# Kernel tuning notes

Hardware: AMD Instinct MI355X
Metric: run time of the kernel (lower is better)

## Reference

```python
import jax, jax.numpy as jnp
import numpy as np

B, N, D, H, DFF, L = 2, 1024, 384, 8, 512, 4
HD = D // H  # 48
RBF_COUNT, RBF_MIN, RBF_MAX = 16, 0.0, 20.0


def layer_norm(x, g, b, eps=1e-5):
    m = jnp.mean(x, axis=-1, keepdims=True)
    v = jnp.var(x, axis=-1, keepdims=True)
    return (x - m) / jnp.sqrt(v + eps) * g + b


def setup_inputs() -> dict:
    key = jax.random.key(0)
    ks = jax.random.split(key, 30)
    rn = lambda k, shape, s=0.02: (jax.random.normal(k, shape, jnp.float32) * s)
    inp = {
        'x_rigid': jax.random.normal(ks[0], (B, N, D), jnp.float32),
        'altered_direction': jax.random.normal(ks[1], (B, N, N, 3), jnp.float32),
        'orientation': jax.random.normal(ks[2], (B, N, N, 3, 3), jnp.float32),
        'distance': jax.random.uniform(ks[3], (B, N, N), jnp.float32) * RBF_MAX,
        'attention_mask': jax.random.randint(ks[4], (B, N, N), 0, 2).astype(jnp.int32),
        'Wq': rn(ks[5], (L, D, D)), 'bq': rn(ks[6], (L, D)),
        'Wk': rn(ks[7], (L, D, D)), 'bk': rn(ks[8], (L, D)),
        'Wv': rn(ks[9], (L, D, D)), 'bv': rn(ks[10], (L, D)),
        'W3': rn(ks[11], (L, D, 3)), 'b3': rn(ks[12], (L, 3)),
        'Wmlp': rn(ks[13], (L, RBF_COUNT), 0.1), 'bmlp': rn(ks[14], (L,), 0.1),
        'Wfc': rn(ks[15], (L, D + 3, D)), 'bfc': rn(ks[16], (L, D)),
        'Wff1': rn(ks[17], (L, D, DFF)), 'bff1': rn(ks[18], (L, DFF)),
        'Wff2': rn(ks[19], (L, DFF, D)), 'bff2': rn(ks[20], (L, D)),
        'ln1_g': jnp.ones((L, D), jnp.float32), 'ln1_b': jnp.zeros((L, D), jnp.float32),
        'ln2_g': jnp.ones((L, D), jnp.float32), 'ln2_b': jnp.zeros((L, D), jnp.float32),
    }
    return inp


def reference(x_rigid, altered_direction, orientation, distance, attention_mask,
              Wq, bq, Wk, bk, Wv, bv, W3, b3, Wmlp, bmlp, Wfc, bfc,
              Wff1, bff1, Wff2, bff2, ln1_g, ln1_b, ln2_g, ln2_b):
    # RBF features of pairwise distance: [B,N,N,16] (shared across layers)
    mu = jnp.linspace(RBF_MIN, RBF_MAX, RBF_COUNT).astype(x_rigid.dtype)
    sigma = (RBF_MAX - RBF_MIN) / RBF_COUNT
    rbf = jnp.exp(-(((distance[..., None] - mu) / sigma) ** 2))
    mask0 = attention_mask == 0  # [B,N,N]
    scale = jnp.sqrt(jnp.asarray(HD, x_rigid.dtype))

    x = x_rigid
    for l in range(L):
        h = layer_norm(x, ln1_g[l], ln1_b[l])
        q = (h @ Wq[l] + bq[l]).reshape(B, N, H, HD).transpose(0, 2, 1, 3)
        k = (h @ Wk[l] + bk[l]).reshape(B, N, H, HD).transpose(0, 2, 1, 3)
        v = (h @ Wv[l] + bv[l]).reshape(B, N, H, HD).transpose(0, 2, 1, 3)
        scores = jnp.einsum('bhqd,bhkd->bhqk', q, k) / scale
        # RBF distance bias via 16->1 linear (head-broadcast, same as repeat+mlp)
        dis = jnp.einsum('bqkr,r->bqk', rbf, Wmlp[l]) + bmlp[l]
        scores = scores + dis[:, None]
        scores = jnp.where(mask0[:, None], jnp.asarray(-1e9, scores.dtype), scores)
        attn = jax.nn.softmax(scores, axis=-1)
        attn_v = jnp.einsum('bhqk,bhkd->bhqd', attn, v)
        attn_v = attn_v.transpose(0, 2, 1, 3).reshape(B, N, D)
        # merged-head softmax drives the geometric frame update
        merged = jax.nn.softmax(jnp.sum(scores, axis=1), axis=-1)  # [B,N,N]
        v3d = h @ W3[l] + b3[l]  # [B,N,3]
        v3d_map = jnp.einsum('bijmn,bjn->bijn', orientation, v3d)  # [B,N,N,3]
        v3d_dir = jnp.cross(altered_direction, v3d_map)  # [B,N,N,3]
        attn_frame = jnp.mean(merged[..., None] * v3d_dir, axis=-2)  # [B,N,3]
        out = jnp.concatenate([attn_v, attn_frame], axis=-1) @ Wfc[l] + bfc[l]
        x = x + out
        h2 = layer_norm(x, ln2_g[l], ln2_b[l])
        x = x + (jax.nn.relu(h2 @ Wff1[l] + bff1[l]) @ Wff2[l] + bff2[l])
    return x
```

## Files before the change

kernel.cpp:

```cpp
#include <hip/hip_runtime.h>
#include <math.h>

constexpr int B_ = 2, N_ = 1024, D_ = 384, H_ = 8, HD_ = 48, DFF2 = 512, L_ = 4;
constexpr int BN_ = B_ * N_;
constexpr size_t NNs = (size_t)N_ * N_;
constexpr size_t BNNc = (size_t)B_ * N_ * N_;
constexpr int JT = 64, NSPLIT = 4;
constexpr int CCLD = 448;
constexpr float RSCALE = 0.14433756729740643f;

typedef short bf16x8 __attribute__((ext_vector_type(8)));
typedef float f32x4 __attribute__((ext_vector_type(4)));

__device__ inline float wsum(float v) {
#pragma unroll
  for (int m = 32; m; m >>= 1) v += __shfl_xor(v, m, 64);
  return v;
}
__device__ inline float b2f(unsigned int s) {
  union { unsigned int u; float f; } v; v.u = s << 16; return v.f;
}
__device__ inline unsigned short f2b(float f) {
  union { float f; unsigned int u; } v; v.f = f;
  unsigned int r = v.u + 0x7fffu + ((v.u >> 16) & 1u);
  return (unsigned short)(r >> 16);
}

__global__ __launch_bounds__(256) void misc_kernel(float* __restrict__ x,
                                                   const float* __restrict__ x_rigid,
                                                   unsigned short* __restrict__ qp,
                                                   unsigned short* __restrict__ kpf,
                                                   const float* __restrict__ bq,
                                                   const float* __restrict__ bk,
                                                   const float* __restrict__ bv,
                                                   float* __restrict__ bqkv) {
  int gid = blockIdx.x * 256 + threadIdx.x;
  if (gid < 786432) { x[gid] = x_rigid[gid]; return; }
  gid -= 786432;
  if (gid < 262144) {
    int r = gid >> 7, rem = gid & 127;
    int h = rem >> 4, c = rem & 15;
    qp[(size_t)r * 512 + h * 64 + 48 + c] = 0;
    return;
  }
  gid -= 262144;
  if (gid < 262144) {
    int fh = gid >> 8, rem = gid & 255;
    kpf[(size_t)fh * 1024 + 768 + rem] = 0;
    return;
  }
  gid -= 262144;
  if (gid < L_ * 1152) {
    int l = gid / 1152, n = gid % 1152;
    bqkv[gid] = (n < 384) ? bq[l * D_ + n] : (n < 768) ? bk[l * D_ + n - 384] : bv[l * D_ + n - 768];
  }
}

__global__ __launch_bounds__(256) void pack_all_kernel(
    const float* __restrict__ Wq, const float* __restrict__ Wk, const float* __restrict__ Wv,
    const float* __restrict__ Wfc, const float* __restrict__ Wff1, const float* __restrict__ Wff2,
    unsigned short* __restrict__ WqkvT, unsigned short* __restrict__ WfcT,
    unsigned short* __restrict__ Wff1T, unsigned short* __restrict__ Wff2T) {
  __shared__ float ts[32][33];
  const int bid = blockIdx.x;
  const int lz = blockIdx.z;
  const int t = threadIdx.x;
  const float* in;
  unsigned short* out;
  size_t istr, ostr;
  int K, Nc, Kpad, n0, k0;
  if (bid < 432) {
    int which = bid / 144, r = bid % 144;
    n0 = (r % 12) * 32; k0 = (r / 12) * 32;
    in = (which == 0) ? Wq : (which == 1) ? Wk : Wv;
    istr = (size_t)D_ * D_;
    out = WqkvT + (size_t)which * 384 * 384;
    ostr = (size_t)1152 * D_;
    K = D_; Nc = D_; Kpad = D_;
  } else if (bid < 600) {
    int r = bid - 432;
    n0 = (r % 12) * 32; k0 = (r / 12) * 32;
    in = Wfc; istr = (size_t)387 * D_;
    out = WfcT; ostr = (size_t)D_ * CCLD;
    K = 387; Nc = D_; Kpad = CCLD;
  } else if (bid < 792) {
    int r = bid - 600;
    n0 = (r % 16) * 32; k0 = (r / 16) * 32;
    in = Wff1; istr = (size_t)D_ * DFF2;
    out = Wff1T; ostr = (size_t)DFF2 * D_;
    K = D_; Nc = DFF2; Kpad = D_;
  } else {
    int r = bid - 792;
    n0 = (r % 12) * 32; k0 = (r / 16 == 0 ? 0 : 0, r / 12) * 32;
    in = Wff2; istr = (size_t)DFF2 * D_;
    out = Wff2T; ostr = (size_t)D_ * DFF2;
    K = DFF2; Nc = D_; Kpad = DFF2;
  }
  const float* inl = in + (size_t)lz * istr;
  unsigned short* outl = out + (size_t)lz * ostr;
#pragma unroll
  for (int u = 0; u < 4; ++u) {
    int i = t + u * 256, kk = i >> 5, nn = i & 31;
    int k = k0 + kk;
    ts[kk][nn] = (k < K) ? inl[(size_t)k * Nc + n0 + nn] : 0.f;
  }
  __syncthreads();
#pragma unroll
  for (int u = 0; u < 4; ++u) {
    int i = t + u * 256, nn = i >> 5, kk = i & 31;
    outl[(size_t)(n0 + nn) * Kpad + k0 + kk] = f2b(ts[kk][nn]);
  }
}

__global__ __launch_bounds__(256) void precomp_kernel(const float* __restrict__ ori,
                                                      const float* __restrict__ ad,
                                                      const float* __restrict__ dist,
                                                      const int* __restrict__ mask,
                                                      const float* __restrict__ Wmlp,
                                                      const float* __restrict__ bmlp,
                                                      uint2* __restrict__ Ga,
                                                      unsigned int* __restrict__ Gz,
                                                      unsigned short* __restrict__ db4) {
  size_t i4 = ((size_t)blockIdx.x * 256 + threadIdx.x) * 4;
  if (i4 >= BNNc) return;
  float ov[36], av[12];
  const float4* op4 = reinterpret_cast<const float4*>(ori + i4 * 9);
#pragma unroll
  for (int u = 0; u < 9; ++u) {
    float4 v = op4[u];
    ov[u * 4 + 0] = v.x; ov[u * 4 + 1] = v.y; ov[u * 4 + 2] = v.z; ov[u * 4 + 3] = v.w;
  }
  const float4* ap4 = reinterpret_cast<const float4*>(ad + i4 * 3);
#pragma unroll
  for (int u = 0; u < 3; ++u) {
    float4 v = ap4[u];
    av[u * 4 + 0] = v.x; av[u * 4 + 1] = v.y; av[u * 4 + 2] = v.z; av[u * 4 + 3] = v.w;
  }
  float4 dv4 = *reinterpret_cast<const float4*>(dist + i4);
  int4 mk4 = *reinterpret_cast<const int4*>(mask + i4);
  float dvs[4] = {dv4.x, dv4.y, dv4.z, dv4.w};
  int mks[4] = {mk4.x, mk4.y, mk4.z, mk4.w};
  uint4 gaout[2];
  unsigned int gzout[4];
#pragma unroll
  for (int e = 0; e < 4; ++e) {
    const float* op = &ov[e * 9];
    const float* ap = &av[e * 3];
    float c0 = op[0] + op[3] + op[6];
    float c1 = op[1] + op[4] + op[7];
    float c2 = op[2] + op[5] + op[8];
    float a0 = ap[0], a1 = ap[1], a2 = ap[2];
    unsigned int w0 = (unsigned int)f2b(a1 * c2) | ((unsigned int)f2b(a2 * c1) << 16);
    unsigned int w1 = (unsigned int)f2b(a2 * c0) | ((unsigned int)f2b(a0 * c2) << 16);
    ((unsigned int*)gaout)[e * 2 + 0] = w0;
    ((unsigned int*)gaout)[e * 2 + 1] = w1;
    gzout[e] = (unsigned int)f2b(a0 * c1) | ((unsigned int)f2b(a1 * c0) << 16);
  }
  *reinterpret_cast<uint4*>(&Ga[i4]) = gaout[0];
  *reinterpret_cast<uint4*>(&Ga[i4 + 2]) = gaout[1];
  *reinterpret_cast<uint4*>(&Gz[i4]) = *reinterpret_cast<uint4*>(gzout);
  float sv[4][4];
#pragma unroll
  for (int e = 0; e < 4; ++e) {
    float rb[16];
#pragma unroll
    for (int r = 0; r < 16; ++r) {
      float tt = (dvs[e] - (float)r * (20.0f / 15.0f)) * 0.8f;
      rb[r] = __expf(-tt * tt);
    }
#pragma unroll
    for (int l2 = 0; l2 < L_; ++l2) {
      float s = bmlp[l2];
#pragma unroll
      for (int r = 0; r < 16; ++r) s += rb[r] * Wmlp[l2 * 16 + r];
      sv[e][l2] = s;
    }
  }
#pragma unroll
  for (int l2 = 0; l2 < L_; ++l2) {
    unsigned int lo = (unsigned int)f2b(mks[0] == 0 ? -1e9f : sv[0][l2]) |
                      ((unsigned int)f2b(mks[1] == 0 ? -1e9f : sv[1][l2]) << 16);
    unsigned int hi = (unsigned int)f2b(mks[2] == 0 ? -1e9f : sv[2][l2]) |
                      ((unsigned int)f2b(mks[3] == 0 ? -1e9f : sv[3][l2]) << 16);
    uint2 w; w.x = lo; w.y = hi;
    *reinterpret_cast<uint2*>(&db4[(size_t)l2 * BNNc + i4]) = w;
  }
}

__global__ __launch_bounds__(256) void geomb_kernel(const float* __restrict__ ori,
                                                    const float* __restrict__ ad,
                                                    uint2* __restrict__ Ga,
                                                    unsigned int* __restrict__ Gz) {
  size_t i = (size_t)blockIdx.x * 256 + threadIdx.x;
  size_t stride = (size_t)gridDim.x * 256;
  for (; i < BNNc; i += stride) {
    const float* op = ori + i * 9;
    const float* ap = ad + i * 3;
    float c0 = op[0] + op[3] + op[6];
    float c1 = op[1] + op[4] + op[7];
    float c2 = op[2] + op[5] + op[8];
    float a0 = ap[0], a1 = ap[1], a2 = ap[2];
    uint2 oa;
    oa.x = (unsigned int)f2b(a1 * c2) | ((unsigned int)f2b(a2 * c1) << 16);
    oa.y = (unsigned int)f2b(a2 * c0) | ((unsigned int)f2b(a0 * c2) << 16);
    Ga[i] = oa;
    Gz[i] = (unsigned int)f2b(a0 * c1) | ((unsigned int)f2b(a1 * c0) << 16);
  }
}
__global__ __launch_bounds__(256) void rbf4_kernel(const float* __restrict__ dist,
                                                   const int* __restrict__ mask,
                                                   const float* __restrict__ Wmlp,
                                                   const float* __restrict__ bmlp,
                                                   unsigned short* __restrict__ db4) {
  size_t i = (size_t)blockIdx.x * 256 + threadIdx.x;
  size_t stride = (size_t)gridDim.x * 256;
  for (; i < BNNc; i += stride) {
    float dv = dist[i];
    bool msk = (mask[i] == 0);
    float rb[16];
#pragma unroll
    for (int r = 0; r < 16; ++r) {
      float tt = (dv - (float)r * (20.0f / 15.0f)) * 0.8f;
      rb[r] = __expf(-tt * tt);
    }
#pragma unroll
    for (int l2 = 0; l2 < L_; ++l2) {
      float sv = bmlp[l2];
#pragma unroll
      for (int r = 0; r < 16; ++r) sv += rb[r] * Wmlp[l2 * 16 + r];
      db4[(size_t)l2 * BNNc + i] = f2b(msk ? -1e9f : sv);
    }
  }
}
__global__ __launch_bounds__(256) void rbf_kernel(const float* __restrict__ dist,
                                                  const int* __restrict__ mask,
                                                  const float* __restrict__ wm,
                                                  const float* __restrict__ bm,
                                                  unsigned short* __restrict__ dbias) {
  size_t i = (size_t)blockIdx.x * 256 + threadIdx.x;
  size_t stride = (size_t)gridDim.x * 256;
  float w[16];
#pragma unroll
  for (int r = 0; r < 16; ++r) w[r] = wm[r];
  float b0 = bm[0];
  for (; i < BNNc; i += stride) {
    float dv = dist[i];
    float sv = b0;
#pragma unroll
    for (int r = 0; r < 16; ++r) {
      float tt = (dv - (float)r * (20.0f / 15.0f)) * 0.8f;
      sv += __expf(-tt * tt) * w[r];
    }
    dbias[i] = f2b((mask[i] == 0) ? -1e9f : sv);
  }
}

template <bool V3D>
__global__ __launch_bounds__(256) void ln_kernel(const float* __restrict__ x,
                                                 const float* __restrict__ g,
                                                 const float* __restrict__ b,
                                                 unsigned short* __restrict__ out,
                                                 const float* __restrict__ W3,
                                                 const float* __restrict__ b3,
                                                 float* __restrict__ v3d) {
  int lane = threadIdx.x & 63, wid = threadIdx.x >> 6;
  int row = blockIdx.x * 4 + wid;
  const float* xp = x + (size_t)row * D_;
  float v[6], s = 0.f, s2 = 0.f;
#pragma unroll
  for (int i = 0; i < 6; ++i) {
    v[i] = xp[lane + i * 64];
    s += v[i]; s2 += v[i] * v[i];
  }
  s = wsum(s); s2 = wsum(s2);
  float mean = s * (1.0f / D_);
  float var = s2 * (1.0f / D_) - mean * mean;
  float rstd = rsqrtf(var + 1e-5f);
  unsigned short* op = out + (size_t)row * D_;
  float a0 = 0.f, a1 = 0.f, a2 = 0.f;
#pragma unroll
  for (int i = 0; i < 6; ++i) {
    int d = lane + i * 64;
    float nv = (v[i] - mean) * rstd * g[d] + b[d];
    op[d] = f2b(nv);
    if (V3D) {
      a0 += nv * W3[d * 3 + 0];
      a1 += nv * W3[d * 3 + 1];
      a2 += nv * W3[d * 3 + 2];
    }
  }
  if (V3D) {
    a0 = wsum(a0); a1 = wsum(a1); a2 = wsum(a2);
    if (lane == 0) {
      v3d[row * 3 + 0] = a0 + b3[0];
      v3d[row * 3 + 1] = a1 + b3[1];
      v3d[row * 3 + 2] = a2 + b3[2];
    }
  }
}

template <int EPI>
__global__ __launch_bounds__(256) void mfma_gemm2(const unsigned short* __restrict__ A, int lda,
                                                  const unsigned short* __restrict__ WT, int ldw,
                                                  const float* __restrict__ bias,
                                                  float* __restrict__ C0, float* __restrict__ C1,
                                                  float* __restrict__ C2, int ldc, int K) {
  __shared__ __align__(16) unsigned short As[2][64 * 72];
  __shared__ __align__(16) unsigned short Bs[2][32 * 72];
  const int t = threadIdx.x;
  const int l = t & 63, w = t >> 6;
  const int lr = l & 15, lk = l >> 4;
  const int n0 = blockIdx.x * 32, m0 = blockIdx.y * 64;
  const int wm = (w & 1) * 32, wn = (w >> 1) * 16;
  const int arow = t >> 3, acol8 = (t & 7) * 8;
  uint4 ra0, ra1, rb;
  const unsigned short* pa0 = A + (size_t)(m0 + arow) * lda + acol8;
  const unsigned short* pa1 = A + (size_t)(m0 + arow + 32) * lda + acol8;
  const unsigned short* pb = WT + (size_t)(n0 + arow) * ldw + acol8;
  ra0 = *reinterpret_cast<const uint4*>(pa0);
  ra1 = *reinterpret_cast<const uint4*>(pa1);
  rb = *reinterpret_cast<const uint4*>(pb);
  f32x4 acc[2] = {};
  int p = 0;
  for (int kt = 0; kt < K; kt += 64) {
    *reinterpret_cast<uint4*>(&As[p][arow * 72 + acol8]) = ra0;
    *reinterpret_cast<uint4*>(&As[p][(arow + 32) * 72 + acol8]) = ra1;
    *reinterpret_cast<uint4*>(&Bs[p][arow * 72 + acol8]) = rb;
    if (kt + 64 < K) {
      ra0 = *reinterpret_cast<const uint4*>(pa0 + kt + 64);
      ra1 = *reinterpret_cast<const uint4*>(pa1 + kt + 64);
      rb = *reinterpret_cast<const uint4*>(pb + kt + 64);
    }
    __syncthreads();
#pragma unroll
    for (int ks = 0; ks < 2; ++ks) {
      bf16x8 av0 = *reinterpret_cast<const bf16x8*>(&As[p][(wm + lr) * 72 + ks * 32 + lk * 8]);
      bf16x8 av1 = *reinterpret_cast<const bf16x8*>(&As[p][(wm + 16 + lr) * 72 + ks * 32 + lk * 8]);
      bf16x8 bv = *reinterpret_cast<const bf16x8*>(&Bs[p][(wn + lr) * 72 + ks * 32 + lk * 8]);
      acc[0] = __builtin_amdgcn_mfma_f32_16x16x32_bf16(av0, bv, acc[0], 0, 0, 0);
      acc[1] = __builtin_amdgcn_mfma_f32_16x16x32_bf16(av1, bv, acc[1], 0, 0, 0);
    }
    p ^= 1;
  }
#pragma unroll
  for (int mi = 0; mi < 2; ++mi)
#pragma unroll
    for (int e = 0; e < 4; ++e) {
      int row = m0 + wm + mi * 16 + lk * 4 + e;
      int col = n0 + wn + lr;
      float v = acc[mi][e] + bias[col];
      if (EPI == 0) {
        if (col < 384) {
          int h = col / 48, hd = col - h * 48;
          ((unsigned short*)C0)[(size_t)row * 512 + h * 64 + hd] = f2b(v * RSCALE);
        } else if (col < 768) {
          int c2 = col - 384;
          int h = c2 / 48, d = c2 - h * 48;
          int b2 = row >> 10, j = row & 1023;
          int jb = j >> 4, jr = j & 15;
          int ks = d >> 5, dd = d & 31;
          size_t fid = (((size_t)(b2 * 64 + jb) * 8 + h) << 1) + ks;
          ((unsigned short*)C1)[fid * 512 + (size_t)(jr + ((dd >> 3) << 4)) * 8 + (d & 7)] = f2b(v);
        } else {
          int d = col - 768;
          int b2 = row >> 10, j = row & 1023;
          int jg = j >> 5, df = d >> 4;
          size_t fid = (size_t)(b2 * 32 + jg) * 24 + df;
          ((unsigned short*)C2)[fid * 512 + (size_t)((d & 15) + (((j & 31) >> 3) << 4)) * 8 + (j & 7)] = f2b(v);
        }
      }
      if (EPI == 1) C0[(size_t)row * ldc + col] += v;
      if (EPI == 2) ((unsigned short*)C0)[(size_t)row * ldc + col] = f2b(fmaxf(v, 0.f));
    }
}

template <bool USEG>
__global__ __launch_bounds__(512, 4) void attn16_kernel(
    const unsigned short* __restrict__ qp, const unsigned short* __restrict__ kpf,
    const unsigned short* __restrict__ vf, const unsigned short* __restrict__ db_l,
    const uint2* __restrict__ Ga, const unsigned int* __restrict__ Gz,
    const float* __restrict__ ad, const float* __restrict__ ori,
    const float* __restrict__ v3d,
    unsigned short* __restrict__ pO, float* __restrict__ pM, float* __restrict__ pL,
    float* __restrict__ pF, float* __restrict__ pMg, float* __restrict__ pLg) {
  __shared__ __align__(16) unsigned short pbuf[8 * 16 * 72];
  __shared__ __align__(16) unsigned short msw[8 * 16 * 68];
  __shared__ __align__(16) float dbs[16 * 68];
  __shared__ float fg_s[16];

  const int t = threadIdx.x;
  const int wv = t >> 6, l = t & 63;
  const int lr = l & 15, lk = l >> 4;
  const int sgrp = blockIdx.y;
  const int i0 = blockIdx.x * 16;
  const int b = i0 >> 10, ib = i0 & 1023;
  const int mr = t >> 5, mc = t & 31;

  const bf16x8 qf0 = *reinterpret_cast<const bf16x8*>(
      qp + (size_t)(i0 + lr) * 512 + wv * 64 + lk * 8);
  const bf16x8 qf1 = *reinterpret_cast<const bf16x8*>(
      qp + (size_t)(i0 + lr) * 512 + wv * 64 + 32 + lk * 8);

  f32x4 Ofr[3] = {};
  float fracc[2][3] = {};
  float m_ph[4], l_ph[4], fhv[4];
#pragma unroll
  for (int e = 0; e < 4; ++e) { m_ph[e] = -INFINITY; l_ph[e] = 0.f; }
  float m_mg = -INFINITY, l_mg = 0.f;

  for (int jt = sgrp * (N_ / NSPLIT); jt < (sgrp + 1) * (N_ / NSPLIT); jt += JT) {
    uint2 ga_r0, ga_r1;
    unsigned int gz_r0, gz_r1;
    float w0p = 0.f, w1p = 0.f, w2p = 0.f;
    if (USEG) {
      const float* vp = v3d + (size_t)((b << 10) + jt + l) * 3;
      w0p = vp[0]; w1p = vp[1]; w2p = vp[2];
      size_t pij0 = ((size_t)b * N_ + (ib + wv * 2)) * N_ + jt + l;
      ga_r0 = Ga[pij0];
      gz_r0 = Gz[pij0];
      ga_r1 = Ga[pij0 + N_];
      gz_r1 = Gz[pij0 + N_];
    }
    if (t < 128) {
      int r = t >> 3, c4 = t & 7;
      const uint4* src = reinterpret_cast<const uint4*>(
                             db_l + (size_t)b * NNs + (size_t)(ib + r) * N_ + jt) + c4;
      uint4 v = *src;
      float* dp = &dbs[r * 68 + c4 * 8];
      dp[0] = b2f(v.x & 0xffffu); dp[1] = b2f(v.x >> 16);
      dp[2] = b2f(v.y & 0xffffu); dp[3] = b2f(v.y >> 16);
      dp[4] = b2f(v.z & 0xffffu); dp[5] = b2f(v.z >> 16);
      dp[6] = b2f(v.w & 0xffffu); dp[7] = b2f(v.w >> 16);
    }
    f32x4 sc[4];
    {
      const unsigned short* kbase =
          kpf + ((((size_t)(b * 64) + (jt >> 4)) * 8 + wv) * 2 * 64 + l) * 8;
      bf16x8 kf0[4], kf1[4];
#pragma unroll
      for (int nj = 0; nj < 4; ++nj) {
        kf0[nj] = *reinterpret_cast<const bf16x8*>(kbase + (size_t)nj * 16 * 512);
        kf1[nj] = *reinterpret_cast<const bf16x8*>(kbase + (size_t)nj * 16 * 512 + 512);
      }
#pragma unroll
      for (int nj = 0; nj < 4; ++nj) {
        f32x4 acc = {};
        acc = __builtin_amdgcn_mfma_f32_16x16x32_bf16(qf0, kf0[nj], acc, 0, 0, 0);
        acc = __builtin_amdgcn_mfma_f32_16x16x32_bf16(qf1, kf1[nj], acc, 0, 0, 0);
        sc[nj] = acc;
      }
    }
#pragma unroll
    for (int nj = 0; nj < 4; ++nj)
#pragma unroll
      for (int e = 0; e < 4; ++e)
        msw[(wv * 16 + lk * 4 + e) * 68 + nj * 16 + lr] = f2b(sc[nj][e]);
    __syncthreads();
    bool needO;
    {
      float sv[4][4];
#pragma unroll
      for (int nj = 0; nj < 4; ++nj)
#pragma unroll
        for (int e = 0; e < 4; ++e)
          sv[nj][e] = sc[nj][e] + dbs[(lk * 4 + e) * 68 + nj * 16 + lr];
      float lm[4];
      bool need = false;
#pragma unroll
      for (int e = 0; e < 4; ++e) {
        lm[e] = fmaxf(fmaxf(sv[0][e], sv[1][e]), fmaxf(sv[2][e], sv[3][e]));
        need = need || (lm[e] > m_ph[e] + 8.f);
      }
      needO = __any(need);
      if (needO) {
#pragma unroll
        for (int e = 0; e < 4; ++e) {
          float rm = lm[e];
          rm = fmaxf(rm, __shfl_xor(rm, 1, 64));
          rm = fmaxf(rm, __shfl_xor(rm, 2, 64));
          rm = fmaxf(rm, __shfl_xor(rm, 4, 64));
          rm = fmaxf(rm, __shfl_xor(rm, 8, 64));
          float nm = fmaxf(m_ph[e], rm);
          fhv[e] = __expf(m_ph[e] - nm);
          m_ph[e] = nm;
          l_ph[e] *= fhv[e];
        }
      }
#pragma unroll
      for (int e = 0; e < 4; ++e) {
        float ls = 0.f;
#pragma unroll
        for (int nj = 0; nj < 4; ++nj) {
          float pv = __expf(sv[nj][e] - m_ph[e]);
          sv[nj][e] = pv;
          ls += pv;
        }
        ls += __shfl_xor(ls, 1, 64);
        ls += __shfl_xor(ls, 2, 64);
        ls += __shfl_xor(ls, 4, 64);
        ls += __shfl_xor(ls, 8, 64);
        l_ph[e] += ls;
#pragma unroll
        for (int nj = 0; nj < 4; ++nj)
          pbuf[(wv * 16 + lk * 4 + e) * 72 + nj * 16 + lr] = f2b(sv[nj][e]);
      }
    }
    {
      float mv[2];
#pragma unroll
      for (int i = 0; i < 2; ++i) {
        int j = mc + 32 * i;
        float s = 8.f * dbs[mr * 68 + j];
#pragma unroll
        for (int h = 0; h < 8; ++h) s += b2f(msw[(h * 16 + mr) * 68 + j]);
        mv[i] = s;
      }
      float lm2 = fmaxf(mv[0], mv[1]);
      bool needm = __any(lm2 > m_mg + 8.f);
      if (needm) {
        float tmax = lm2;
        tmax = fmaxf(tmax, __shfl_xor(tmax, 1, 64));
        tmax = fmaxf(tmax, __shfl_xor(tmax, 2, 64));
        tmax = fmaxf(tmax, __shfl_xor(tmax, 4, 64));
        tmax = fmaxf(tmax, __shfl_xor(tmax, 8, 64));
        tmax = fmaxf(tmax, __shfl_xor(tmax, 16, 64));
        float nm = fmaxf(m_mg, tmax);
        float f = __expf(m_mg - nm);
        m_mg = nm;
        l_mg *= f;
        if (mc == 0) fg_s[mr] = f;
      } else if (mc == 0) {
        fg_s[mr] = 1.f;
      }
      float lsum = 0.f;
#pragma unroll
      for (int i = 0; i < 2; ++i) {
        mv[i] = __expf(mv[i] - m_mg);
        lsum += mv[i];
        msw[mr * 68 + mc + 32 * i] = f2b(mv[i]);
      }
      lsum += __shfl_xor(lsum, 1, 64);
      lsum += __shfl_xor(lsum, 2, 64);
      lsum += __shfl_xor(lsum, 4, 64);
      lsum += __shfl_xor(lsum, 8, 64);
      lsum += __shfl_xor(lsum, 16, 64);
      l_mg += lsum;
    }
    {
      bf16x8 af0 = *reinterpret_cast<const bf16x8*>(&pbuf[(wv * 16 + lr) * 72 + lk * 8]);
      bf16x8 af1 = *reinterpret_cast<const bf16x8*>(&pbuf[(wv * 16 + lr) * 72 + 32 + lk * 8]);
      const unsigned short* vbase =
          vf + ((((size_t)(b * 32) + (jt >> 5)) * 24 + wv * 3) * 64 + l) * 8;
#pragma unroll
      for (int ni = 0; ni < 3; ++ni) {
        bf16x8 bf0 = *reinterpret_cast<const bf16x8*>(vbase + (size_t)ni * 512);
        bf16x8 bf1 = *reinterpret_cast<const bf16x8*>(vbase + (size_t)(24 + ni) * 512);
        f32x4 o = Ofr[ni];
        if (needO) {
#pragma unroll
          for (int e = 0; e < 4; ++e) o[e] *= fhv[e];
        }
        o = __builtin_amdgcn_mfma_f32_16x16x32_bf16(af0, bf0, o, 0, 0, 0);
        o = __builtin_amdgcn_mfma_f32_16x16x32_bf16(af1, bf1, o, 0, 0, 0);
        Ofr[ni] = o;
      }
    }
    {
      float w0, w1, w2;
      if (USEG) {
        w0 = w0p; w1 = w1p; w2 = w2p;
      } else {
        const float* vp = v3d + (size_t)((b << 10) + jt + l) * 3;
        w0 = vp[0]; w1 = vp[1]; w2 = vp[2];
      }
#pragma unroll
      for (int e = 0; e < 2; ++e) {
        int r = wv * 2 + e;
        float pm = b2f(msw[r * 68 + l]);
        float d0, d1, d2;
        if (USEG) {
          uint2 ga = (e == 0) ? ga_r0 : ga_r1;
          unsigned int gz = (e == 0) ? gz_r0 : gz_r1;
          float g0 = b2f(ga.x & 0xffffu), g1 = b2f(ga.x >> 16);
          float g2 = b2f(ga.y & 0xffffu), g3 = b2f(ga.y >> 16);
          float g4 = b2f(gz & 0xffffu), g5 = b2f(gz >> 16);
          d0 = g0 * w2 - g1 * w1;
          d1 = g2 * w0 - g3 * w2;
          d2 = g4 * w1 - g5 * w0;
        } else {
          size_t pij = ((size_t)b * N_ + (ib + r)) * N_ + jt + l;
          const float* op = ori + pij * 9;
          const float* ap = ad + pij * 3;
          float a0 = ap[0], a1 = ap[1], a2 = ap[2];
          float u0 = (op[0] + op[3] + op[6]) * w0;
          float u1 = (op[1] + op[4] + op[7]) * w1;
          float u2 = (op[2] + op[5] + op[8]) * w2;
          d0 = a1 * u2 - a2 * u1; d1 = a2 * u0 - a0 * u2; d2 = a0 * u1 - a1 * u0;
        }
        float fgr = fg_s[r];
        fracc[e][0] = fracc[e][0] * fgr + pm * d0;
        fracc[e][1] = fracc[e][1] * fgr + pm * d1;
        fracc[e][2] = fracc[e][2] * fgr + pm * d2;
      }
    }
    __syncthreads();
  }
  const size_t rowb = (size_t)sgrp * BN_ + i0;
#pragma unroll
  for (int ni = 0; ni < 3; ++ni)
#pragma unroll
    for (int e = 0; e < 4; ++e)
      pO[(rowb + lk * 4 + e) * D_ + wv * 48 + ni * 16 + lr] = f2b(Ofr[ni][e]);
#pragma unroll
  for (int e = 0; e < 2; ++e)
#pragma unroll
    for (int c = 0; c < 3; ++c) {
      float v = wsum(fracc[e][c]);
      if (l == 0) pF[(rowb + wv * 2 + e) * 3 + c] = v;
    }
  if (lr == 0) {
#pragma unroll
    for (int e = 0; e < 4; ++e) {
      pM[(rowb + lk * 4 + e) * H_ + wv] = m_ph[e];
      pL[(rowb + lk * 4 + e) * H_ + wv] = l_ph[e];
    }
  }
  if (mc == 0) { pMg[rowb + mr] = m_mg; pLg[rowb + mr] = l_mg; }
}

constexpr int QR = 8;
__global__ __launch_bounds__(256) void combine_kernel(
    const unsigned short* __restrict__ pO, const float* __restrict__ pM,
    const float* __restrict__ pL, const float* __restrict__ pF,
    const float* __restrict__ pMg, const float* __restrict__ pLg,
    unsigned short* __restrict__ cc) {
  __shared__ float sc[QR][H_][NSPLIT];
  __shared__ float scg[QR][NSPLIT];
  int t = threadIdx.x;
  int i0 = blockIdx.x * QR;
  if (t < QR * H_) {
    int r = t >> 3, h = t & 7;
    size_t row = i0 + r;
    float ms[NSPLIT], ls[NSPLIT], m = -INFINITY;
#pragma unroll
    for (int s2 = 0; s2 < NSPLIT; ++s2) {
      ms[s2] = pM[((size_t)s2 * BN_ + row) * H_ + h];
      ls[s2] = pL[((size_t)s2 * BN_ + row) * H_ + h];
      m = fmaxf(m, ms[s2]);
    }
    float L = 0.f, e[NSPLIT];
#pragma unroll
    for (int s2 = 0; s2 < NSPLIT; ++s2) { e[s2] = __expf(ms[s2] - m); L += ls[s2] * e[s2]; }
    float invL = 1.0f / L;
#pragma unroll
    for (int s2 = 0; s2 < NSPLIT; ++s2) sc[r][h][s2] = e[s2] * invL;
  } else if (t < QR * H_ + QR) {
    int r = t - QR * H_;
    size_t row = i0 + r;
    float ms[NSPLIT], ls[NSPLIT], m = -INFINITY;
#pragma unroll
    for (int s2 = 0; s2 < NSPLIT; ++s2) {
      ms[s2] = pMg[(size_t)s2 * BN_ + row];
      ls[s2] = pLg[(size_t)s2 * BN_ + row];
      m = fmaxf(m, ms[s2]);
    }
    float L = 0.f, e[NSPLIT];
#pragma unroll
    for (int s2 = 0; s2 < NSPLIT; ++s2) { e[s2] = __expf(ms[s2] - m); L += ls[s2] * e[s2]; }
    float inv = 1.0f / (L * (float)N_);
#pragma unroll
    for (int s2 = 0; s2 < NSPLIT; ++s2) scg[r][s2] = e[s2] * inv;
  }
  __syncthreads();
#pragma unroll
  for (int r = 0; r < QR; ++r) {
    size_t row = i0 + r;
    for (int d = t; d < D_; d += 256) {
      int h = d / HD_;
      float o = 0.f;
#pragma unroll
      for (int s2 = 0; s2 < NSPLIT; ++s2)
        o += b2f(pO[((size_t)s2 * BN_ + row) * D_ + d]) * sc[r][h][s2];
      cc[row * CCLD + d] = f2b(o);
    }
  }
  if (t < QR * 3) {
    int r = t / 3, c = t % 3;
    size_t row = i0 + r;
    float F = 0.f;
#pragma unroll
    for (int s2 = 0; s2 < NSPLIT; ++s2) F += pF[((size_t)s2 * BN_ + row) * 3 + c] * scg[r][s2];
    cc[row * CCLD + 384 + c] = f2b(F);
  }
  for (int idx = t; idx < QR * (CCLD - 387); idx += 256) {
    int r = idx / (CCLD - 387), col = 387 + idx % (CCLD - 387);
    cc[(size_t)(i0 + r) * CCLD + col] = 0;
  }
}

extern "C" void kernel_launch(void* const* d_in, const int* in_sizes, int n_in,
                              void* d_out, int out_size, void* d_ws, size_t ws_size,
                              hipStream_t stream) {
  const float* x_rigid = (const float*)d_in[0];
  const float* ad      = (const float*)d_in[1];
  const float* ori     = (const float*)d_in[2];
  const float* dist    = (const float*)d_in[3];
  const int*   mask    = (const int*)d_in[4];
  const float* Wq  = (const float*)d_in[5];
  const float* bq  = (const float*)d_in[6];
  const float* Wk  = (const float*)d_in[7];
  const float* bk  = (const float*)d_in[8];
  const float* Wv  = (const float*)d_in[9];
  const float* bv  = (const float*)d_in[10];
  const float* W3  = (const float*)d_in[11];
  const float* b3  = (const float*)d_in[12];
  const float* Wmlp = (const float*)d_in[13];
  const float* bmlp = (const float*)d_in[14];
  const float* Wfc  = (const float*)d_in[15];
  const float* bfc  = (const float*)d_in[16];
  const float* Wff1 = (const float*)d_in[17];
  const float* bff1 = (const float*)d_in[18];
  const float* Wff2 = (const float*)d_in[19];
  const float* bff2 = (const float*)d_in[20];
  const float* ln1g = (const float*)d_in[21];
  const float* ln1b = (const float*)d_in[22];
  const float* ln2g = (const float*)d_in[23];
  const float* ln2b = (const float*)d_in[24];

  float* x = (float*)d_out;

  size_t off = 0;
  auto alloc = [&](size_t bytes) -> void* {
    void* r = (char*)d_ws + off;
    off = (off + bytes + 255) & ~(size_t)255;
    return r;
  };
  unsigned short* WqkvT = (unsigned short*)alloc((size_t)L_ * 1152 * D_ * 2);
  unsigned short* WfcT  = (unsigned short*)alloc((size_t)L_ * D_ * CCLD * 2);
  unsigned short* Wff1T = (unsigned short*)alloc((size_t)L_ * DFF2 * D_ * 2);
  unsigned short* Wff2T = (unsigned short*)alloc((size_t)L_ * D_ * DFF2 * 2);
  float* bqkv = (float*)alloc((size_t)L_ * 1152 * 4);
  unsigned short* qp  = (unsigned short*)alloc((size_t)BN_ * 512 * 2);
  unsigned short* kpf = (unsigned short*)alloc((size_t)2048 * 64 * 8 * 2);
  unsigned short* vf  = (unsigned short*)alloc((size_t)1536 * 64 * 8 * 2);
  unsigned short* hb  = (unsigned short*)alloc((size_t)BN_ * D_ * 2);
  unsigned short* h2  = (unsigned short*)alloc((size_t)BN_ * D_ * 2);
  unsigned short* cc  = (unsigned short*)alloc((size_t)BN_ * CCLD * 2);
  unsigned short* ffb = (unsigned short*)alloc((size_t)BN_ * DFF2 * 2);
  float* v3 = (float*)alloc((size_t)BN_ * 3 * 4);
  unsigned short* pO = (unsigned short*)alloc((size_t)NSPLIT * BN_ * D_ * 2);
  float* pM = (float*)alloc((size_t)NSPLIT * BN_ * H_ * 4);
  float* pL = (float*)alloc((size_t)NSPLIT * BN_ * H_ * 4);
  float* pF = (float*)alloc((size_t)NSPLIT * BN_ * 3 * 4);
  float* pMg = (float*)alloc((size_t)NSPLIT * BN_ * 4);
  float* pLg = (float*)alloc((size_t)NSPLIT * BN_ * 4);
  size_t need_base = off;
  uint2* Ga = (uint2*)alloc(BNNc * 8);
  unsigned int* Gz = (unsigned int*)alloc(BNNc * 4);
  bool useG = (off <= ws_size);
  size_t off_g = useG ? off : need_base;
  off = off_g;
  unsigned short* db4 = (unsigned short*)alloc((size_t)L_ * BNNc * 2);
  bool use4 = (off <= ws_size);
  unsigned short* db1 = nullptr;
  if (!use4) {
    off = off_g;
    db1 = (unsigned short*)alloc(BNNc * 2);
    if (off > ws_size) return;
  }
  if (ws_size < need_base) return;

  pack_all_kernel<<<dim3(984, 1, L_), 256, 0, stream>>>(Wq, Wk, Wv, Wfc, Wff1, Wff2,
                                                        WqkvT, WfcT, Wff1T, Wff2T);
  misc_kernel<<<5138, 256, 0, stream>>>(x, x_rigid, qp, kpf, bq, bk, bv, bqkv);
  if (useG && use4) {
    precomp_kernel<<<2048, 256, 0, stream>>>(ori, ad, dist, mask, Wmlp, bmlp, Ga, Gz, db4);
  } else {
    if (useG) geomb_kernel<<<4096, 256, 0, stream>>>(ori, ad, Ga, Gz);
    if (use4) rbf4_kernel<<<4096, 256, 0, stream>>>(dist, mask, Wmlp, bmlp, db4);
  }

  for (int l = 0; l < L_; ++l) {
    const unsigned short* db_l = use4 ? (db4 + (size_t)l * BNNc) : db1;
    if (!use4) rbf_kernel<<<4096, 256, 0, stream>>>(dist, mask, Wmlp + l * 16, bmlp + l, db1);
    ln_kernel<true><<<BN_ / 4, 256, 0, stream>>>(x, ln1g + l * D_, ln1b + l * D_, hb,
                                                 W3 + (size_t)l * D_ * 3, b3 + l * 3, v3);
    mfma_gemm2<0><<<dim3(36, 32), 256, 0, stream>>>(
        hb, D_, WqkvT + (size_t)l * 1152 * D_, D_, bqkv + l * 1152,
        (float*)qp, (float*)kpf, (float*)vf, 0, D_);
    if (useG)
      attn16_kernel<true><<<dim3(BN_ / 16, NSPLIT), 512, 0, stream>>>(
          qp, kpf, vf, db_l, Ga, Gz, ad, ori, v3, pO, pM, pL, pF, pMg, pLg);
    else
      attn16_kernel<false><<<dim3(BN_ / 16, NSPLIT), 512, 0, stream>>>(
          qp, kpf, vf, db_l, Ga, Gz, ad, ori, v3, pO, pM, pL, pF, pMg, pLg);
    combine_kernel<<<BN_ / QR, 256, 0, stream>>>(pO, pM, pL, pF, pMg, pLg, cc);
    mfma_gemm2<1><<<dim3(12, 32), 256, 0, stream>>>(
        cc, CCLD, WfcT + (size_t)l * D_ * CCLD, CCLD, bfc + l * D_, x, nullptr, nullptr, D_, CCLD);
    ln_kernel<false><<<BN_ / 4, 256, 0, stream>>>(x, ln2g + l * D_, ln2b + l * D_, h2,
                                                  nullptr, nullptr, nullptr);
    mfma_gemm2<2><<<dim3(16, 32), 256, 0, stream>>>(
        h2, D_, Wff1T + (size_t)l * DFF2 * D_, D_, bff1 + l * DFF2, (float*)ffb, nullptr, nullptr,
        DFF2, D_);
    mfma_gemm2<1><<<dim3(12, 32), 256, 0, stream>>>(
        ffb, DFF2, Wff2T + (size_t)l * D_ * DFF2, DFF2, bff2 + l * D_, x, nullptr, nullptr, D_,
        DFF2);
  }
}
```

Measured before the change: 319.7 us.

## Fuse geometry precompute into first-layer attention and drop separate precomp pass

Removes the geometry part of the standalone precompute kernel. The first layer's attention kernel now reads orientation and direction directly, and while doing so writes the packed bf16 Ga/Gz terms for the later layers to reuse. This avoids one extra full pass over the large orientation and direction tensors. In exchange, the layer-0 attention kernel takes on extra global stores and raw fp32 loads, which can lengthen its critical path. Layer 0 also now uses fp32 geometry products rather than bf16-rounded ones, so its results differ slightly from later layers.

```diff
diff --git a/kernel.cpp b/kernel.cpp
--- a/kernel.cpp
+++ b/kernel.cpp
@@ -91,7 +91,7 @@
     K = D_; Nc = DFF2; Kpad = D_;
   } else {
     int r = bid - 792;
-    n0 = (r % 12) * 32; k0 = (r / 16 == 0 ? 0 : 0, r / 12) * 32;
+    n0 = (r % 12) * 32; k0 = (r / 12) * 32;
     in = Wff2; istr = (size_t)DFF2 * D_;
     out = Wff2T; ostr = (size_t)D_ * DFF2;
     K = DFF2; Nc = D_; Kpad = DFF2;
@@ -112,53 +112,17 @@
   }
 }
 
-__global__ __launch_bounds__(256) void precomp_kernel(const float* __restrict__ ori,
-                                                      const float* __restrict__ ad,
-                                                      const float* __restrict__ dist,
-                                                      const int* __restrict__ mask,
-                                                      const float* __restrict__ Wmlp,
-                                                      const float* __restrict__ bmlp,
-                                                      uint2* __restrict__ Ga,
-                                                      unsigned int* __restrict__ Gz,
-                                                      unsigned short* __restrict__ db4) {
+__global__ __launch_bounds__(256) void rbf4v_kernel(const float* __restrict__ dist,
+                                                    const int* __restrict__ mask,
+                                                    const float* __restrict__ Wmlp,
+                                                    const float* __restrict__ bmlp,
+                                                    unsigned short* __restrict__ db4) {
   size_t i4 = ((size_t)blockIdx.x * 256 + threadIdx.x) * 4;
   if (i4 >= BNNc) return;
-  float ov[36], av[12];
-  const float4* op4 = reinterpret_cast<const float4*>(ori + i4 * 9);
-#pragma unroll
-  for (int u = 0; u < 9; ++u) {
-    float4 v = op4[u];
-    ov[u * 4 + 0] = v.x; ov[u * 4 + 1] = v.y; ov[u * 4 + 2] = v.z; ov[u * 4 + 3] = v.w;
-  }
-  const float4* ap4 = reinterpret_cast<const float4*>(ad + i4 * 3);
-#pragma unroll
-  for (int u = 0; u < 3; ++u) {
-    float4 v = ap4[u];
-    av[u * 4 + 0] = v.x; av[u * 4 + 1] = v.y; av[u * 4 + 2] = v.z; av[u * 4 + 3] = v.w;
-  }
   float4 dv4 = *reinterpret_cast<const float4*>(dist + i4);
   int4 mk4 = *reinterpret_cast<const int4*>(mask + i4);
   float dvs[4] = {dv4.x, dv4.y, dv4.z, dv4.w};
   int mks[4] = {mk4.x, mk4.y, mk4.z, mk4.w};
-  uint4 gaout[2];
-  unsigned int gzout[4];
-#pragma unroll
-  for (int e = 0; e < 4; ++e) {
-    const float* op = &ov[e * 9];
-    const float* ap = &av[e * 3];
-    float c0 = op[0] + op[3] + op[6];
-    float c1 = op[1] + op[4] + op[7];
-    float c2 = op[2] + op[5] + op[8];
-    float a0 = ap[0], a1 = ap[1], a2 = ap[2];
-    unsigned int w0 = (unsigned int)f2b(a1 * c2) | ((unsigned int)f2b(a2 * c1) << 16);
-    unsigned int w1 = (unsigned int)f2b(a2 * c0) | ((unsigned int)f2b(a0 * c2) << 16);
-    ((unsigned int*)gaout)[e * 2 + 0] = w0;
-    ((unsigned int*)gaout)[e * 2 + 1] = w1;
-    gzout[e] = (unsigned int)f2b(a0 * c1) | ((unsigned int)f2b(a1 * c0) << 16);
-  }
-  *reinterpret_cast<uint4*>(&Ga[i4]) = gaout[0];
-  *reinterpret_cast<uint4*>(&Ga[i4 + 2]) = gaout[1];
-  *reinterpret_cast<uint4*>(&Gz[i4]) = *reinterpret_cast<uint4*>(gzout);
   float sv[4][4];
 #pragma unroll
   for (int e = 0; e < 4; ++e) {
@@ -184,52 +148,6 @@
                       ((unsigned int)f2b(mks[3] == 0 ? -1e9f : sv[3][l2]) << 16);
     uint2 w; w.x = lo; w.y = hi;
     *reinterpret_cast<uint2*>(&db4[(size_t)l2 * BNNc + i4]) = w;
-  }
-}
-
-__global__ __launch_bounds__(256) void geomb_kernel(const float* __restrict__ ori,
-                                                    const float* __restrict__ ad,
-                                                    uint2* __restrict__ Ga,
-                                                    unsigned int* __restrict__ Gz) {
-  size_t i = (size_t)blockIdx.x * 256 + threadIdx.x;
-  size_t stride = (size_t)gridDim.x * 256;
-  for (; i < BNNc; i += stride) {
-    const float* op = ori + i * 9;
-    const float* ap = ad + i * 3;
-    float c0 = op[0] + op[3] + op[6];
-    float c1 = op[1] + op[4] + op[7];
-    float c2 = op[2] + op[5] + op[8];
-    float a0 = ap[0], a1 = ap[1], a2 = ap[2];
-    uint2 oa;
-    oa.x = (unsigned int)f2b(a1 * c2) | ((unsigned int)f2b(a2 * c1) << 16);
-    oa.y = (unsigned int)f2b(a2 * c0) | ((unsigned int)f2b(a0 * c2) << 16);
-    Ga[i] = oa;
-    Gz[i] = (unsigned int)f2b(a0 * c1) | ((unsigned int)f2b(a1 * c0) << 16);
-  }
-}
-__global__ __launch_bounds__(256) void rbf4_kernel(const float* __restrict__ dist,
-                                                   const int* __restrict__ mask,
-                                                   const float* __restrict__ Wmlp,
-                                                   const float* __restrict__ bmlp,
-                                                   unsigned short* __restrict__ db4) {
-  size_t i = (size_t)blockIdx.x * 256 + threadIdx.x;
-  size_t stride = (size_t)gridDim.x * 256;
-  for (; i < BNNc; i += stride) {
-    float dv = dist[i];
-    bool msk = (mask[i] == 0);
-    float rb[16];
-#pragma unroll
-    for (int r = 0; r < 16; ++r) {
-      float tt = (dv - (float)r * (20.0f / 15.0f)) * 0.8f;
-      rb[r] = __expf(-tt * tt);
-    }
-#pragma unroll
-    for (int l2 = 0; l2 < L_; ++l2) {
-      float sv = bmlp[l2];
-#pragma unroll
-      for (int r = 0; r < 16; ++r) sv += rb[r] * Wmlp[l2 * 16 + r];
-      db4[(size_t)l2 * BNNc + i] = f2b(msk ? -1e9f : sv);
-    }
   }
 }
 __global__ __launch_bounds__(256) void rbf_kernel(const float* __restrict__ dist,
@@ -374,11 +292,11 @@
     }
 }
 
-template <bool USEG>
+template <int GMODE>
 __global__ __launch_bounds__(512, 4) void attn16_kernel(
     const unsigned short* __restrict__ qp, const unsigned short* __restrict__ kpf,
     const unsigned short* __restrict__ vf, const unsigned short* __restrict__ db_l,
-    const uint2* __restrict__ Ga, const unsigned int* __restrict__ Gz,
+    uint2* __restrict__ Ga, unsigned int* __restrict__ Gz,
     const float* __restrict__ ad, const float* __restrict__ ori,
     const float* __restrict__ v3d,
     unsigned short* __restrict__ pO, float* __restrict__ pM, float* __restrict__ pL,
@@ -412,7 +330,7 @@
     uint2 ga_r0, ga_r1;
     unsigned int gz_r0, gz_r1;
     float w0p = 0.f, w1p = 0.f, w2p = 0.f;
-    if (USEG) {
+    if (GMODE == 1) {
       const float* vp = v3d + (size_t)((b << 10) + jt + l) * 3;
       w0p = vp[0]; w1p = vp[1]; w2p = vp[2];
       size_t pij0 = ((size_t)b * N_ + (ib + wv * 2)) * N_ + jt + l;
@@ -567,7 +485,7 @@
     }
     {
       float w0, w1, w2;
-      if (USEG) {
+      if (GMODE == 1) {
         w0 = w0p; w1 = w1p; w2 = w2p;
       } else {
         const float* vp = v3d + (size_t)((b << 10) + jt + l) * 3;
@@ -578,7 +496,7 @@
         int r = wv * 2 + e;
         float pm = b2f(msw[r * 68 + l]);
         float d0, d1, d2;
-        if (USEG) {
+        if (GMODE == 1) {
           uint2 ga = (e == 0) ? ga_r0 : ga_r1;
           unsigned int gz = (e == 0) ? gz_r0 : gz_r1;
           float g0 = b2f(ga.x & 0xffffu), g1 = b2f(ga.x >> 16);
@@ -592,10 +510,21 @@
           const float* op = ori + pij * 9;
           const float* ap = ad + pij * 3;
           float a0 = ap[0], a1 = ap[1], a2 = ap[2];
-          float u0 = (op[0] + op[3] + op[6]) * w0;
-          float u1 = (op[1] + op[4] + op[7]) * w1;
-          float u2 = (op[2] + op[5] + op[8]) * w2;
-          d0 = a1 * u2 - a2 * u1; d1 = a2 * u0 - a0 * u2; d2 = a0 * u1 - a1 * u0;
+          float c0 = op[0] + op[3] + op[6];
+          float c1 = op[1] + op[4] + op[7];
+          float c2 = op[2] + op[5] + op[8];
+          float g0 = a1 * c2, g1 = a2 * c1, g2 = a2 * c0;
+          float g3 = a0 * c2, g4 = a0 * c1, g5 = a1 * c0;
+          d0 = g0 * w2 - g1 * w1;
+          d1 = g2 * w0 - g3 * w2;
+          d2 = g4 * w1 - g5 * w0;
+          if (GMODE == 0) {
+            uint2 oa;
+            oa.x = (unsigned int)f2b(g0) | ((unsigned int)f2b(g1) << 16);
+            oa.y = (unsigned int)f2b(g2) | ((unsigned int)f2b(g3) << 16);
+            Ga[pij] = oa;
+            Gz[pij] = (unsigned int)f2b(g4) | ((unsigned int)f2b(g5) << 16);
+          }
         }
         float fgr = fg_s[r];
         fracc[e][0] = fracc[e][0] * fgr + pm * d0;
@@ -773,12 +702,7 @@
   pack_all_kernel<<<dim3(984, 1, L_), 256, 0, stream>>>(Wq, Wk, Wv, Wfc, Wff1, Wff2,
                                                         WqkvT, WfcT, Wff1T, Wff2T);
   misc_kernel<<<5138, 256, 0, stream>>>(x, x_rigid, qp, kpf, bq, bk, bv, bqkv);
-  if (useG && use4) {
-    precomp_kernel<<<2048, 256, 0, stream>>>(ori, ad, dist, mask, Wmlp, bmlp, Ga, Gz, db4);
-  } else {
-    if (useG) geomb_kernel<<<4096, 256, 0, stream>>>(ori, ad, Ga, Gz);
-    if (use4) rbf4_kernel<<<4096, 256, 0, stream>>>(dist, mask, Wmlp, bmlp, db4);
-  }
+  if (use4) rbf4v_kernel<<<2048, 256, 0, stream>>>(dist, mask, Wmlp, bmlp, db4);
 
   for (int l = 0; l < L_; ++l) {
     const unsigned short* db_l = use4 ? (db4 + (size_t)l * BNNc) : db1;
@@ -788,11 +712,14 @@
     mfma_gemm2<0><<<dim3(36, 32), 256, 0, stream>>>(
         hb, D_, WqkvT + (size_t)l * 1152 * D_, D_, bqkv + l * 1152,
         (float*)qp, (float*)kpf, (float*)vf, 0, D_);
-    if (useG)
-      attn16_kernel<true><<<dim3(BN_ / 16, NSPLIT), 512, 0, stream>>>(
+    if (!useG)
+      attn16_kernel<2><<<dim3(BN_ / 16, NSPLIT), 512, 0, stream>>>(
+          qp, kpf, vf, db_l, Ga, Gz, ad, ori, v3, pO, pM, pL, pF, pMg, pLg);
+    else if (l == 0)
+      attn16_kernel<0><<<dim3(BN_ / 16, NSPLIT), 512, 0, stream>>>(
           qp, kpf, vf, db_l, Ga, Gz, ad, ori, v3, pO, pM, pL, pF, pMg, pLg);
     else
-      attn16_kernel<false><<<dim3(BN_ / 16, NSPLIT), 512, 0, stream>>>(
+      attn16_kernel<1><<<dim3(BN_ / 16, NSPLIT), 512, 0, stream>>>(
           qp, kpf, vf, db_l, Ga, Gz, ad, ori, v3, pO, pM, pL, pF, pMg, pLg);
     combine_kernel<<<BN_ / QR, 256, 0, stream>>>(pO, pM, pL, pF, pMg, pLg, cc);
     mfma_gemm2<1><<<dim3(12, 32), 256, 0, stream>>>(
```

New measurement: 326.4 us. +2.1%, slower.
